# Optimization experiments

Measured on AMD Instinct MI355X. Metric: run time of the kernel, lower is better.

The kernel has to match this reference:

```python
import jax, jax.numpy as jnp
import numpy as np

D = 256
H = 8
DIM = D // H
NL = 8  # number of layers
LAYER_NAMES = ["self", "cross", "self", "cross", "self", "cross", "self", "cross"]
EPS_ATTN = 1e-6
EPS_LN = 1e-5


def setup_inputs() -> dict:
    key = jax.random.key(0)
    ks = jax.random.split(key, 16)
    B, L = 8, 4800
    s = 1.0 / np.sqrt(D)
    inp = {
        "desc0": jax.random.normal(ks[0], (B, L, D), jnp.float32),
        "desc1": jax.random.normal(ks[1], (B, L, D), jnp.float32),
        "mask0": jnp.ones((B, L), jnp.float32),
        "mask1": jnp.ones((B, L), jnp.float32),
        # shared LinearAttention params (one instance reused by all layers)
        "Wq": jax.random.normal(ks[2], (D, D), jnp.float32) * s,
        "bq": jnp.zeros((D,), jnp.float32),
        "Wk": jax.random.normal(ks[3], (D, D), jnp.float32) * s,
        "bk": jnp.zeros((D,), jnp.float32),
        "Wv": jax.random.normal(ks[4], (D, D), jnp.float32) * s,
        "bv": jnp.zeros((D,), jnp.float32),
        "Wm": jax.random.normal(ks[5], (D, D), jnp.float32) * s,
        "bm": jnp.zeros((D,), jnp.float32),
        # per-layer MLP (no bias) and layernorm params, stacked over layers
        "w1": jax.random.normal(ks[6], (NL, D, 2 * D), jnp.float32) * s,
        "w2": jax.random.normal(ks[7], (NL, 2 * D, D), jnp.float32) * (1.0 / np.sqrt(2 * D)),
        "g1": jnp.ones((NL, D), jnp.float32),
        "b1": jnp.zeros((NL, D), jnp.float32),
        "g2": jnp.ones((NL, D), jnp.float32),
        "b2": jnp.zeros((NL, D), jnp.float32),
    }
    return inp


def _layernorm(x, g, b):
    mu = jnp.mean(x, axis=-1, keepdims=True)
    var = jnp.mean(jnp.square(x - mu), axis=-1, keepdims=True)
    return (x - mu) * jax.lax.rsqrt(var + EPS_LN) * g + b


def _linear_attention(q_in, k_in, v_in, qmask, kmask, Wq, bq, Wk, bk, Wv, bv, Wm, bm):
    B, L, _ = q_in.shape
    Q = (q_in @ Wq + bq).reshape(B, -1, H, DIM)
    K = (k_in @ Wk + bk).reshape(B, -1, H, DIM)
    V = (v_in @ Wv + bv).reshape(B, -1, H, DIM)
    Q = jax.nn.elu(Q) + 1.0
    K = jax.nn.elu(K) + 1.0
    Q = Q * qmask[:, :, None, None]
    K = K * kmask[:, :, None, None]
    V = V * kmask[:, :, None, None]
    KV = jnp.einsum("nshd,nshm->nhmd", K, V)          # [B,H,DIM,DIM]
    Z = 1.0 / (jnp.einsum("nlhd,nhd->nlh", Q, K.sum(axis=1)) + EPS_ATTN)
    out = jnp.einsum("nlhd,nhmd,nlh->nlhm", Q, KV, Z)  # [B,L,H,DIM]
    return out.reshape(B, L, D) @ Wm + bm


def _layer(x, source, xmask, smask, Wq, bq, Wk, bk, Wv, bv, Wm, bm, w1, w2, g1, b1, g2, b2):
    msg = _linear_attention(x, source, source, xmask, smask, Wq, bq, Wk, bk, Wv, bv, Wm, bm)
    msg = _layernorm(msg, g1, b1)
    msg = jax.nn.relu(msg @ w1) @ w2
    msg = _layernorm(msg, g2, b2)
    return x + msg


def reference(desc0, desc1, mask0, mask1, Wq, bq, Wk, bk, Wv, bv, Wm, bm, w1, w2, g1, b1, g2, b2):
    attn = (Wq, bq, Wk, bk, Wv, bv, Wm, bm)
    for i, name in enumerate(LAYER_NAMES):
        lp = (w1[i], w2[i], g1[i], b1[i], g2[i], b2[i])
        if name == "self":
            desc0 = _layer(desc0, desc0, mask0, mask0, *attn, *lp)
            desc1 = _layer(desc1, desc1, mask1, mask1, *attn, *lp)
        else:
            desc0 = _layer(desc0, desc1, mask0, mask1, *attn, *lp)
            desc1 = _layer(desc1, desc0, mask1, mask0, *attn, *lp)
    return (desc0, desc1)
```

## Files before the change

kernel.cpp:

```cpp
#include <hip/hip_runtime.h>
#include <hip/hip_bf16.h>

typedef __attribute__((ext_vector_type(8))) short short8;
typedef __attribute__((ext_vector_type(4))) float f32x4;

#define NROWS 38400
#define LSEQ 4800
#define BATCH 8
#define NHEAD 8

__device__ inline float b2f(ushort u) {
  union { ushort s; __hip_bfloat16 h; } c;
  c.s = u;
  return __bfloat162float(c.h);
}
__device__ inline ushort f2b(float f) {
  union { ushort s; __hip_bfloat16 h; } c;
  c.h = __float2bfloat16(f);
  return c.s;
}

__device__ inline void gll16(const void* g, void* l) {
  __builtin_amdgcn_global_load_lds(
      (const __attribute__((address_space(1))) void*)g,
      (__attribute__((address_space(3))) void*)l, 16, 0, 0);
}

__global__ __launch_bounds__(256) void transpose_bf16(
    const float* __restrict__ src, __hip_bfloat16* __restrict__ dst, int R, int C) {
  src += (size_t)blockIdx.z * R * C;
  dst += (size_t)blockIdx.z * R * C;
  __shared__ float tile[32][33];
  int bx = blockIdx.x, by = blockIdx.y;
  int tx = threadIdx.x & 31, ty = threadIdx.x >> 5;
  for (int rr = ty; rr < 32; rr += 8)
    tile[rr][tx] = src[(long)(by * 32 + rr) * C + bx * 32 + tx];
  __syncthreads();
  for (int rr = ty; rr < 32; rr += 8)
    dst[(long)(bx * 32 + rr) * R + by * 32 + tx] = __float2bfloat16(tile[tx][rr]);
}

__global__ __launch_bounds__(256) void init_x(
    const float* __restrict__ d0, const float* __restrict__ d1,
    float* __restrict__ outF, __hip_bfloat16* __restrict__ X0b,
    __hip_bfloat16* __restrict__ X1b, long n) {
  long i = (long)blockIdx.x * 256 + threadIdx.x;
  if (i < n) {
    float a = d0[i], b = d1[i];
    outF[i] = a;
    outF[n + i] = b;
    X0b[i] = __float2bfloat16(a);
    X1b[i] = __float2bfloat16(b);
  }
}

#define BM 128
#define BN 128
#define BKK 64

__global__ __launch_bounds__(256) void gemm_bt(
    const __hip_bfloat16* __restrict__ A, const __hip_bfloat16* __restrict__ Bt,
    const float* __restrict__ bias, const float* __restrict__ rowmask,
    __hip_bfloat16* __restrict__ C, int M, int Nout, int K, int act) {
  __shared__ alignas(16) char smem[128 * 136 * 2];
  __hip_bfloat16 (*As)[64] = (__hip_bfloat16(*)[64])smem;
  __hip_bfloat16 (*Bs)[64] = (__hip_bfloat16(*)[64])(smem + 128 * 64 * 2);
  ushort (*Cs)[136] = (ushort(*)[136])smem;

  int tid = threadIdx.x;
  int wave = tid >> 6, lane = tid & 63;
  int wm = wave & 1, wn = wave >> 1;
  int quad = lane >> 4, l16 = lane & 15;
  long mbase = (long)blockIdx.y * BM;
  long nbase = (long)blockIdx.x * BN;

  int srow = lane >> 3;
  int sck = (lane & 7) ^ srow;
  int cx = l16 & 7;

  f32x4 acc[4][4];
#pragma unroll
  for (int i = 0; i < 4; i++)
#pragma unroll
    for (int j = 0; j < 4; j++) acc[i][j] = (f32x4){0.f, 0.f, 0.f, 0.f};

  for (int kt = 0; kt < K; kt += BKK) {
    __syncthreads();
#pragma unroll
    for (int i = 0; i < 4; i++) {
      int r0 = wave * 32 + i * 8;
      gll16(A + (mbase + r0 + srow) * (long)K + kt + sck * 8, &As[r0][0]);
      gll16(Bt + (nbase + r0 + srow) * (long)K + kt + sck * 8, &Bs[r0][0]);
    }
    __syncthreads();
#pragma unroll
    for (int ks = 0; ks < BKK; ks += 32) {
      short8 af[4], bfr[4];
      int ch = ((ks >> 3) + quad) ^ cx;
#pragma unroll
      for (int mt = 0; mt < 4; mt++)
        af[mt] = *(const short8*)&As[wm * 64 + mt * 16 + l16][ch * 8];
#pragma unroll
      for (int nt = 0; nt < 4; nt++)
        bfr[nt] = *(const short8*)&Bs[wn * 64 + nt * 16 + l16][ch * 8];
#pragma unroll
      for (int mt = 0; mt < 4; mt++)
#pragma unroll
        for (int nt = 0; nt < 4; nt++)
          acc[mt][nt] = __builtin_amdgcn_mfma_f32_16x16x32_bf16(
              af[mt], bfr[nt], acc[mt][nt], 0, 0, 0);
    }
  }

  __syncthreads();
#pragma unroll
  for (int nt = 0; nt < 4; nt++) {
    int colt = wn * 64 + nt * 16 + l16;
    float bv = bias ? bias[nbase + colt] : 0.0f;
#pragma unroll
    for (int mt = 0; mt < 4; mt++) {
      int rowt0 = wm * 64 + mt * 16 + quad * 4;
#pragma unroll
      for (int r = 0; r < 4; r++) {
        int rowt = rowt0 + r;
        float v = acc[mt][nt][r] + bv;
        if (act == 1) v = v > 0.f ? v + 1.f : __expf(v);
        else if (act == 2) v = v > 0.f ? v : 0.f;
        if (rowmask) v *= rowmask[mbase + rowt];
        Cs[rowt][colt] = f2b(v);
      }
    }
  }
  __syncthreads();
#pragma unroll
  for (int it = 0; it < 8; it++) {
    int idx = tid + it * 256;
    int row = idx >> 4, c = idx & 15;
    uint4 v = *(const uint4*)&Cs[row][c * 8];
    *(uint4*)(C + (mbase + row) * (long)Nout + nbase + c * 8) = v;
  }
}

__global__ __launch_bounds__(256) void kv_reduce(
    const __hip_bfloat16* __restrict__ Kp, const __hip_bfloat16* __restrict__ Vp,
    float* __restrict__ KV, float* __restrict__ Ksum) {
  int b = blockIdx.x, h = blockIdx.y, c = blockIdx.z;
  __shared__ float Kl[32][40], Vl[32][40];
  int t = threadIdx.x;
  int lrow = t >> 3, le = (t & 7) * 4;
  int d = t >> 3, mg = t & 7;
  float a0 = 0.f, a1 = 0.f, a2 = 0.f, a3 = 0.f, ks = 0.f;
  int base = c * 480;
  for (int st = 0; st < 15; st++) {
    int s0 = base + st * 32;
    __syncthreads();
    {
      long n = (long)b * LSEQ + s0 + lrow;
      ushort4 ku = *(const ushort4*)(Kp + n * 256 + h * 32 + le);
      ushort4 vu = *(const ushort4*)(Vp + n * 256 + h * 32 + le);
      float4 kf = {b2f(ku.x), b2f(ku.y), b2f(ku.z), b2f(ku.w)};
      float4 vf = {b2f(vu.x), b2f(vu.y), b2f(vu.z), b2f(vu.w)};
      *(float4*)&Kl[lrow][le] = kf;
      *(float4*)&Vl[lrow][le] = vf;
    }
    __syncthreads();
#pragma unroll
    for (int ss = 0; ss < 32; ss++) {
      float kd = Kl[ss][d];
      float4 v4 = *(const float4*)&Vl[ss][mg * 4];
      a0 += kd * v4.x; a1 += kd * v4.y; a2 += kd * v4.z; a3 += kd * v4.w;
      if (mg == 0) ks += kd;
    }
  }
  int bh = b * 8 + h;
  float* p = KV + ((long)bh * 32 + d) * 32 + mg * 4;
  atomicAdd(&p[0], a0); atomicAdd(&p[1], a1);
  atomicAdd(&p[2], a2); atomicAdd(&p[3], a3);
  if (mg == 0) atomicAdd(&Ksum[bh * 32 + d], ks);
}

__global__ __launch_bounds__(256) void attn_out(
    const __hip_bfloat16* __restrict__ Qp, const float* __restrict__ KV,
    const float* __restrict__ Ksum, __hip_bfloat16* __restrict__ O) {
  int b = blockIdx.y, h = blockIdx.z;
  int bh = b * 8 + h;
  __shared__ float KVl[32][36];
  int t = threadIdx.x;
  for (int i = t; i < 1024; i += 256) KVl[i >> 5][i & 31] = KV[((long)bh << 10) + i];
  int lane = t & 63, wave = t >> 6;
  int cg = lane & 7, rs = lane >> 3;
  float4 ksr = *(const float4*)&Ksum[bh * 32 + cg * 4];
  __syncthreads();

  int rowEnd = blockIdx.x * 192 + 192;
  for (int r = blockIdx.x * 192 + wave * 8 + rs; r < rowEnd; r += 32) {
    long n = (long)b * LSEQ + r;
    ushort4 qu = *(const ushort4*)(Qp + n * 256 + h * 32 + cg * 4);
    float q0 = b2f(qu.x), q1 = b2f(qu.y), q2 = b2f(qu.z), q3 = b2f(qu.w);
    float den = q0 * ksr.x + q1 * ksr.y + q2 * ksr.z + q3 * ksr.w;
    den += __shfl_xor(den, 1);
    den += __shfl_xor(den, 2);
    den += __shfl_xor(den, 4);
    float s0 = 0.f, s1 = 0.f, s2 = 0.f, s3 = 0.f;
    int gbase = lane & ~7;
#pragma unroll
    for (int j = 0; j < 8; j++) {
      int src = gbase | j;
      float qa = __shfl(q0, src);
      float qb = __shfl(q1, src);
      float qc = __shfl(q2, src);
      float qd = __shfl(q3, src);
      float4 k0 = *(const float4*)&KVl[j * 4 + 0][cg * 4];
      float4 k1 = *(const float4*)&KVl[j * 4 + 1][cg * 4];
      float4 k2 = *(const float4*)&KVl[j * 4 + 2][cg * 4];
      float4 k3 = *(const float4*)&KVl[j * 4 + 3][cg * 4];
      s0 += qa * k0.x + qb * k1.x + qc * k2.x + qd * k3.x;
      s1 += qa * k0.y + qb * k1.y + qc * k2.y + qd * k3.y;
      s2 += qa * k0.z + qb * k1.z + qc * k2.z + qd * k3.z;
      s3 += qa * k0.w + qb * k1.w + qc * k2.w + qd * k3.w;
    }
    float inv = 1.0f / (den + 1e-6f);
    ushort4 ou = {f2b(s0 * inv), f2b(s1 * inv), f2b(s2 * inv), f2b(s3 * inv)};
    *(ushort4*)(O + n * 256 + h * 32 + cg * 4) = ou;
  }
}

__global__ __launch_bounds__(256) void ln_kernel(
    __hip_bfloat16* __restrict__ X, const float* __restrict__ g,
    const float* __restrict__ bt) {
  int wave = threadIdx.x >> 6, lane = threadIdx.x & 63;
  long row = (long)blockIdx.x * 4 + wave;
  __hip_bfloat16* p = X + row * 256 + lane * 4;
  ushort4 u = *(const ushort4*)p;
  float v[4] = {b2f(u.x), b2f(u.y), b2f(u.z), b2f(u.w)};
  float s = v[0] + v[1] + v[2] + v[3];
  float s2 = v[0] * v[0] + v[1] * v[1] + v[2] * v[2] + v[3] * v[3];
#pragma unroll
  for (int off = 32; off; off >>= 1) {
    s += __shfl_xor(s, off);
    s2 += __shfl_xor(s2, off);
  }
  float mu = s * (1.f / 256.f);
  float var = s2 * (1.f / 256.f) - mu * mu;
  float rs = rsqrtf(var + 1e-5f);
  ushort4 o;
  o.x = f2b((v[0] - mu) * rs * g[lane * 4 + 0] + bt[lane * 4 + 0]);
  o.y = f2b((v[1] - mu) * rs * g[lane * 4 + 1] + bt[lane * 4 + 1]);
  o.z = f2b((v[2] - mu) * rs * g[lane * 4 + 2] + bt[lane * 4 + 2]);
  o.w = f2b((v[3] - mu) * rs * g[lane * 4 + 3] + bt[lane * 4 + 3]);
  *(ushort4*)p = o;
}

__global__ __launch_bounds__(256) void final_kernel(
    const __hip_bfloat16* __restrict__ M2, const float* __restrict__ g,
    const float* __restrict__ bt, float* __restrict__ outF,
    __hip_bfloat16* __restrict__ Xb) {
  int wave = threadIdx.x >> 6, lane = threadIdx.x & 63;
  long row = (long)blockIdx.x * 4 + wave;
  const __hip_bfloat16* p = M2 + row * 256 + lane * 4;
  ushort4 u = *(const ushort4*)p;
  float v[4] = {b2f(u.x), b2f(u.y), b2f(u.z), b2f(u.w)};
  float s = v[0] + v[1] + v[2] + v[3];
  float s2 = v[0] * v[0] + v[1] * v[1] + v[2] * v[2] + v[3] * v[3];
#pragma unroll
  for (int off = 32; off; off >>= 1) {
    s += __shfl_xor(s, off);
    s2 += __shfl_xor(s2, off);
  }
  float mu = s * (1.f / 256.f);
  float var = s2 * (1.f / 256.f) - mu * mu;
  float rs = rsqrtf(var + 1e-5f);
  float* op = outF + row * 256 + lane * 4;
  float4 rv = *(float4*)op;
  float r0 = rv.x + ((v[0] - mu) * rs * g[lane * 4 + 0] + bt[lane * 4 + 0]);
  float r1 = rv.y + ((v[1] - mu) * rs * g[lane * 4 + 1] + bt[lane * 4 + 1]);
  float r2 = rv.z + ((v[2] - mu) * rs * g[lane * 4 + 2] + bt[lane * 4 + 2]);
  float r3 = rv.w + ((v[3] - mu) * rs * g[lane * 4 + 3] + bt[lane * 4 + 3]);
  *(float4*)op = (float4){r0, r1, r2, r3};
  ushort4 xb = {f2b(r0), f2b(r1), f2b(r2), f2b(r3)};
  *(ushort4*)(Xb + row * 256 + lane * 4) = xb;
}

extern "C" void kernel_launch(void* const* d_in, const int* in_sizes, int n_in,
                              void* d_out, int out_size, void* d_ws, size_t ws_size,
                              hipStream_t stream) {
  const float* desc0 = (const float*)d_in[0];
  const float* desc1 = (const float*)d_in[1];
  const float* mask0 = (const float*)d_in[2];
  const float* mask1 = (const float*)d_in[3];
  const float* Wq = (const float*)d_in[4];
  const float* bq = (const float*)d_in[5];
  const float* Wk = (const float*)d_in[6];
  const float* bk = (const float*)d_in[7];
  const float* Wv = (const float*)d_in[8];
  const float* bv = (const float*)d_in[9];
  const float* Wm = (const float*)d_in[10];
  const float* bm = (const float*)d_in[11];
  const float* w1 = (const float*)d_in[12];
  const float* w2 = (const float*)d_in[13];
  const float* g1 = (const float*)d_in[14];
  const float* b1 = (const float*)d_in[15];
  const float* g2 = (const float*)d_in[16];
  const float* b2 = (const float*)d_in[17];

  char* ws = (char*)d_ws;
  auto alloc = [&](size_t bytes) {
    char* p = ws;
    ws += (bytes + 255) & ~(size_t)255;
    return p;
  };
  __hip_bfloat16* WqT = (__hip_bfloat16*)alloc(256 * 256 * 2);
  __hip_bfloat16* WkT = (__hip_bfloat16*)alloc(256 * 256 * 2);
  __hip_bfloat16* WvT = (__hip_bfloat16*)alloc(256 * 256 * 2);
  __hip_bfloat16* WmT = (__hip_bfloat16*)alloc(256 * 256 * 2);
  __hip_bfloat16* w1T = (__hip_bfloat16*)alloc((size_t)8 * 512 * 256 * 2);
  __hip_bfloat16* w2T = (__hip_bfloat16*)alloc((size_t)8 * 256 * 512 * 2);
  __hip_bfloat16* X0b = (__hip_bfloat16*)alloc((size_t)NROWS * 256 * 2);
  __hip_bfloat16* X1b = (__hip_bfloat16*)alloc((size_t)NROWS * 256 * 2);
  __hip_bfloat16* Qb = (__hip_bfloat16*)alloc((size_t)NROWS * 256 * 2);
  __hip_bfloat16* Kb = (__hip_bfloat16*)alloc((size_t)NROWS * 256 * 2);
  __hip_bfloat16* Vb = (__hip_bfloat16*)alloc((size_t)NROWS * 256 * 2);
  __hip_bfloat16* Ab = (__hip_bfloat16*)alloc((size_t)NROWS * 256 * 2);
  __hip_bfloat16* H1b = (__hip_bfloat16*)alloc((size_t)NROWS * 512 * 2);
  float* KVws = (float*)alloc((64 * 1024 + 64 * 32) * 4);
  float* Ksum = KVws + 64 * 1024;

  transpose_bf16<<<dim3(8, 8, 1), 256, 0, stream>>>(Wq, WqT, 256, 256);
  transpose_bf16<<<dim3(8, 8, 1), 256, 0, stream>>>(Wk, WkT, 256, 256);
  transpose_bf16<<<dim3(8, 8, 1), 256, 0, stream>>>(Wv, WvT, 256, 256);
  transpose_bf16<<<dim3(8, 8, 1), 256, 0, stream>>>(Wm, WmT, 256, 256);
  transpose_bf16<<<dim3(16, 8, 8), 256, 0, stream>>>(w1, w1T, 256, 512);
  transpose_bf16<<<dim3(8, 16, 8), 256, 0, stream>>>(w2, w2T, 512, 256);

  long nElem = (long)NROWS * 256;
  init_x<<<(nElem + 255) / 256, 256, 0, stream>>>(desc0, desc1, (float*)d_out,
                                                  X0b, X1b, nElem);

  auto gemm = [&](const __hip_bfloat16* A, const __hip_bfloat16* Bt,
                  const float* bias, const float* rm, __hip_bfloat16* C,
                  int Nout, int K, int act) {
    dim3 grid(Nout / BN, NROWS / BM);
    gemm_bt<<<grid, 256, 0, stream>>>(A, Bt, bias, rm, C, NROWS, Nout, K, act);
  };

  auto layer = [&](int x, int s, int i) {
    __hip_bfloat16* Xx = x ? X1b : X0b;
    __hip_bfloat16* Xs = s ? X1b : X0b;
    const float* mx = x ? mask1 : mask0;
    const float* ms = s ? mask1 : mask0;
    gemm(Xx, WqT, bq, mx, Qb, 256, 256, 1);
    gemm(Xs, WkT, bk, ms, Kb, 256, 256, 1);
    gemm(Xs, WvT, bv, ms, Vb, 256, 256, 0);
    hipMemsetAsync(KVws, 0, (64 * 1024 + 64 * 32) * 4, stream);
    kv_reduce<<<dim3(BATCH, NHEAD, 10), 256, 0, stream>>>(Kb, Vb, KVws, Ksum);
    attn_out<<<dim3(25, BATCH, NHEAD), 256, 0, stream>>>(Qb, KVws, Ksum, Ab);
    gemm(Ab, WmT, bm, nullptr, Kb, 256, 256, 0);
    ln_kernel<<<NROWS / 4, 256, 0, stream>>>(Kb, g1 + i * 256, b1 + i * 256);
    gemm(Kb, w1T + (size_t)i * 512 * 256, nullptr, nullptr, H1b, 512, 256, 2);
    gemm(H1b, w2T + (size_t)i * 256 * 512, nullptr, nullptr, Vb, 256, 512, 0);
    final_kernel<<<NROWS / 4, 256, 0, stream>>>(
        Vb, g2 + i * 256, b2 + i * 256, (float*)d_out + (size_t)x * nElem, Xx);
  };

  for (int i = 0; i < 8; i++) {
    if (i % 2 == 0) {
      layer(0, 0, i);
      layer(1, 1, i);
    } else {
      layer(0, 1, i);
      layer(1, 0, i);
    }
  }
}
```

Measured before the change: 3.549 ms.

## Fuse QKV projections and fold layernorms into GEMM epilogues

Concatenates Wq/Wk/Wv into one transposed weight so Q, K and V are produced by a single GEMM launch for self layers (two launches for cross layers), writing an interleaved 768-wide buffer. The Wm projection and the w2 projection get full-row 64x256 tile GEMMs whose epilogues compute layernorm, and for the final one also the residual add and bf16 copy. This removes the separate ln_kernel and final_kernel passes and their round trips through global memory. It also vectorises init_x. In exchange, the LN GEMMs use a grid of only 600 blocks, and their B tile is reloaded for every 64-row block, which may hurt occupancy and GEMM efficiency.

```diff
diff --git a/kernel.cpp b/kernel.cpp
--- a/kernel.cpp
+++ b/kernel.cpp
@@ -8,6 +8,7 @@
 #define LSEQ 4800
 #define BATCH 8
 #define NHEAD 8
+#define QKV_LD 768
 
 __device__ inline float b2f(ushort u) {
   union { ushort s; __hip_bfloat16 h; } c;
@@ -43,25 +44,26 @@
 __global__ __launch_bounds__(256) void init_x(
     const float* __restrict__ d0, const float* __restrict__ d1,
     float* __restrict__ outF, __hip_bfloat16* __restrict__ X0b,
-    __hip_bfloat16* __restrict__ X1b, long n) {
+    __hip_bfloat16* __restrict__ X1b, long n4) {
   long i = (long)blockIdx.x * 256 + threadIdx.x;
-  if (i < n) {
-    float a = d0[i], b = d1[i];
-    outF[i] = a;
-    outF[n + i] = b;
-    X0b[i] = __float2bfloat16(a);
-    X1b[i] = __float2bfloat16(b);
-  }
-}
-
-#define BM 128
-#define BN 128
-#define BKK 64
-
-__global__ __launch_bounds__(256) void gemm_bt(
+  if (i < n4) {
+    float4 a = ((const float4*)d0)[i];
+    float4 b = ((const float4*)d1)[i];
+    ((float4*)outF)[i] = a;
+    ((float4*)outF)[n4 + i] = b;
+    ushort4 ua = {f2b(a.x), f2b(a.y), f2b(a.z), f2b(a.w)};
+    ushort4 ub = {f2b(b.x), f2b(b.y), f2b(b.z), f2b(b.w)};
+    ((ushort4*)X0b)[i] = ua;
+    ((ushort4*)X1b)[i] = ub;
+  }
+}
+
+__global__ __launch_bounds__(256) void gemm_qkv(
     const __hip_bfloat16* __restrict__ A, const __hip_bfloat16* __restrict__ Bt,
-    const float* __restrict__ bias, const float* __restrict__ rowmask,
-    __hip_bfloat16* __restrict__ C, int M, int Nout, int K, int act) {
+    __hip_bfloat16* __restrict__ C, int col0,
+    const float* __restrict__ bq, const float* __restrict__ bk,
+    const float* __restrict__ bv, const float* __restrict__ mq,
+    const float* __restrict__ mkv) {
   __shared__ alignas(16) char smem[128 * 136 * 2];
   __hip_bfloat16 (*As)[64] = (__hip_bfloat16(*)[64])smem;
   __hip_bfloat16 (*Bs)[64] = (__hip_bfloat16(*)[64])(smem + 128 * 64 * 2);
@@ -71,8 +73,8 @@
   int wave = tid >> 6, lane = tid & 63;
   int wm = wave & 1, wn = wave >> 1;
   int quad = lane >> 4, l16 = lane & 15;
-  long mbase = (long)blockIdx.y * BM;
-  long nbase = (long)blockIdx.x * BN;
+  long mbase = (long)blockIdx.y * 128;
+  int nbase = blockIdx.x * 128;
 
   int srow = lane >> 3;
   int sck = (lane & 7) ^ srow;
@@ -84,17 +86,17 @@
 #pragma unroll
     for (int j = 0; j < 4; j++) acc[i][j] = (f32x4){0.f, 0.f, 0.f, 0.f};
 
-  for (int kt = 0; kt < K; kt += BKK) {
+  for (int kt = 0; kt < 256; kt += 64) {
     __syncthreads();
 #pragma unroll
     for (int i = 0; i < 4; i++) {
       int r0 = wave * 32 + i * 8;
-      gll16(A + (mbase + r0 + srow) * (long)K + kt + sck * 8, &As[r0][0]);
-      gll16(Bt + (nbase + r0 + srow) * (long)K + kt + sck * 8, &Bs[r0][0]);
-    }
-    __syncthreads();
-#pragma unroll
-    for (int ks = 0; ks < BKK; ks += 32) {
+      gll16(A + (mbase + r0 + srow) * 256 + kt + sck * 8, &As[r0][0]);
+      gll16(Bt + (long)(nbase + r0 + srow) * 256 + kt + sck * 8, &Bs[r0][0]);
+    }
+    __syncthreads();
+#pragma unroll
+    for (int ks = 0; ks < 64; ks += 32) {
       short8 af[4], bfr[4];
       int ch = ((ks >> 3) + quad) ^ cx;
 #pragma unroll
@@ -113,20 +115,25 @@
   }
 
   __syncthreads();
+  int gc0 = col0 + nbase;
 #pragma unroll
   for (int nt = 0; nt < 4; nt++) {
     int colt = wn * 64 + nt * 16 + l16;
-    float bv = bias ? bias[nbase + colt] : 0.0f;
+    int gcol = gc0 + colt;
+    int seg = gcol >> 8;
+    int ci = gcol & 255;
+    float bvv = (seg == 0) ? bq[ci] : (seg == 1) ? bk[ci] : bv[ci];
+    const float* mask = (seg == 0) ? mq : mkv;
+    bool doelu = seg < 2;
 #pragma unroll
     for (int mt = 0; mt < 4; mt++) {
       int rowt0 = wm * 64 + mt * 16 + quad * 4;
 #pragma unroll
       for (int r = 0; r < 4; r++) {
         int rowt = rowt0 + r;
-        float v = acc[mt][nt][r] + bv;
-        if (act == 1) v = v > 0.f ? v + 1.f : __expf(v);
-        else if (act == 2) v = v > 0.f ? v : 0.f;
-        if (rowmask) v *= rowmask[mbase + rowt];
+        float v = acc[mt][nt][r] + bvv;
+        if (doelu) v = v > 0.f ? v + 1.f : __expf(v);
+        v *= mask[mbase + rowt];
         Cs[rowt][colt] = f2b(v);
       }
     }
@@ -137,13 +144,331 @@
     int idx = tid + it * 256;
     int row = idx >> 4, c = idx & 15;
     uint4 v = *(const uint4*)&Cs[row][c * 8];
-    *(uint4*)(C + (mbase + row) * (long)Nout + nbase + c * 8) = v;
+    *(uint4*)(C + (mbase + row) * (long)QKV_LD + gc0 + c * 8) = v;
+  }
+}
+
+__global__ __launch_bounds__(256) void gemm_w1(
+    const __hip_bfloat16* __restrict__ A, const __hip_bfloat16* __restrict__ Bt,
+    __hip_bfloat16* __restrict__ C) {
+  __shared__ alignas(16) char smem[128 * 136 * 2];
+  __hip_bfloat16 (*As)[64] = (__hip_bfloat16(*)[64])smem;
+  __hip_bfloat16 (*Bs)[64] = (__hip_bfloat16(*)[64])(smem + 128 * 64 * 2);
+  ushort (*Cs)[136] = (ushort(*)[136])smem;
+
+  int tid = threadIdx.x;
+  int wave = tid >> 6, lane = tid & 63;
+  int wm = wave & 1, wn = wave >> 1;
+  int quad = lane >> 4, l16 = lane & 15;
+  long mbase = (long)blockIdx.y * 128;
+  int nbase = blockIdx.x * 128;
+
+  int srow = lane >> 3;
+  int sck = (lane & 7) ^ srow;
+  int cx = l16 & 7;
+
+  f32x4 acc[4][4];
+#pragma unroll
+  for (int i = 0; i < 4; i++)
+#pragma unroll
+    for (int j = 0; j < 4; j++) acc[i][j] = (f32x4){0.f, 0.f, 0.f, 0.f};
+
+  for (int kt = 0; kt < 256; kt += 64) {
+    __syncthreads();
+#pragma unroll
+    for (int i = 0; i < 4; i++) {
+      int r0 = wave * 32 + i * 8;
+      gll16(A + (mbase + r0 + srow) * 256 + kt + sck * 8, &As[r0][0]);
+      gll16(Bt + (long)(nbase + r0 + srow) * 256 + kt + sck * 8, &Bs[r0][0]);
+    }
+    __syncthreads();
+#pragma unroll
+    for (int ks = 0; ks < 64; ks += 32) {
+      short8 af[4], bfr[4];
+      int ch = ((ks >> 3) + quad) ^ cx;
+#pragma unroll
+      for (int mt = 0; mt < 4; mt++)
+        af[mt] = *(const short8*)&As[wm * 64 + mt * 16 + l16][ch * 8];
+#pragma unroll
+      for (int nt = 0; nt < 4; nt++)
+        bfr[nt] = *(const short8*)&Bs[wn * 64 + nt * 16 + l16][ch * 8];
+#pragma unroll
+      for (int mt = 0; mt < 4; mt++)
+#pragma unroll
+        for (int nt = 0; nt < 4; nt++)
+          acc[mt][nt] = __builtin_amdgcn_mfma_f32_16x16x32_bf16(
+              af[mt], bfr[nt], acc[mt][nt], 0, 0, 0);
+    }
+  }
+
+  __syncthreads();
+#pragma unroll
+  for (int nt = 0; nt < 4; nt++) {
+    int colt = wn * 64 + nt * 16 + l16;
+#pragma unroll
+    for (int mt = 0; mt < 4; mt++) {
+      int rowt0 = wm * 64 + mt * 16 + quad * 4;
+#pragma unroll
+      for (int r = 0; r < 4; r++) {
+        float v = acc[mt][nt][r];
+        Cs[rowt0 + r][colt] = f2b(v > 0.f ? v : 0.f);
+      }
+    }
+  }
+  __syncthreads();
+#pragma unroll
+  for (int it = 0; it < 8; it++) {
+    int idx = tid + it * 256;
+    int row = idx >> 4, c = idx & 15;
+    uint4 v = *(const uint4*)&Cs[row][c * 8];
+    *(uint4*)(C + (mbase + row) * 512L + nbase + c * 8) = v;
+  }
+}
+
+__global__ __launch_bounds__(256) void gemm_ln(
+    const __hip_bfloat16* __restrict__ A, const __hip_bfloat16* __restrict__ Bt,
+    const float* __restrict__ bias, const float* __restrict__ g,
+    const float* __restrict__ bln, __hip_bfloat16* __restrict__ C) {
+  __shared__ alignas(16) char smem[8192 + 32768];
+  __hip_bfloat16 (*As)[64] = (__hip_bfloat16(*)[64])smem;
+  __hip_bfloat16 (*Bs)[64] = (__hip_bfloat16(*)[64])(smem + 8192);
+  ushort (*Cs)[264] = (ushort(*)[264])smem;
+  __shared__ float pS[4][64], pS2[4][64], muA[64], rsA[64];
+
+  int tid = threadIdx.x;
+  int wave = tid >> 6, lane = tid & 63;
+  int wn = wave;
+  int quad = lane >> 4, l16 = lane & 15;
+  long mbase = (long)blockIdx.x * 64;
+
+  int srow = lane >> 3;
+  int sck = (lane & 7) ^ srow;
+  int cx = l16 & 7;
+
+  f32x4 acc[4][4];
+#pragma unroll
+  for (int i = 0; i < 4; i++)
+#pragma unroll
+    for (int j = 0; j < 4; j++) acc[i][j] = (f32x4){0.f, 0.f, 0.f, 0.f};
+
+  for (int kt = 0; kt < 256; kt += 64) {
+    __syncthreads();
+#pragma unroll
+    for (int j = 0; j < 2; j++) {
+      int r0 = wave * 16 + j * 8;
+      gll16(A + (mbase + r0 + srow) * 256 + kt + sck * 8, &As[r0][0]);
+    }
+#pragma unroll
+    for (int j = 0; j < 8; j++) {
+      int r0 = wave * 64 + j * 8;
+      gll16(Bt + (r0 + srow) * 256 + kt + sck * 8, &Bs[r0][0]);
+    }
+    __syncthreads();
+#pragma unroll
+    for (int ks = 0; ks < 64; ks += 32) {
+      short8 af[4], bfr[4];
+      int ch = ((ks >> 3) + quad) ^ cx;
+#pragma unroll
+      for (int mt = 0; mt < 4; mt++)
+        af[mt] = *(const short8*)&As[mt * 16 + l16][ch * 8];
+#pragma unroll
+      for (int nt = 0; nt < 4; nt++)
+        bfr[nt] = *(const short8*)&Bs[wn * 64 + nt * 16 + l16][ch * 8];
+#pragma unroll
+      for (int mt = 0; mt < 4; mt++)
+#pragma unroll
+        for (int nt = 0; nt < 4; nt++)
+          acc[mt][nt] = __builtin_amdgcn_mfma_f32_16x16x32_bf16(
+              af[mt], bfr[nt], acc[mt][nt], 0, 0, 0);
+    }
+  }
+
+  float br[4], gr[4], blr[4];
+#pragma unroll
+  for (int nt = 0; nt < 4; nt++) {
+    int gcol = wn * 64 + nt * 16 + l16;
+    br[nt] = bias[gcol];
+    gr[nt] = g[gcol];
+    blr[nt] = bln[gcol];
+  }
+#pragma unroll
+  for (int mt = 0; mt < 4; mt++)
+#pragma unroll
+    for (int r = 0; r < 4; r++) {
+      float s = 0.f, s2 = 0.f;
+#pragma unroll
+      for (int nt = 0; nt < 4; nt++) {
+        float v = acc[mt][nt][r] + br[nt];
+        s += v;
+        s2 += v * v;
+      }
+      s += __shfl_xor(s, 1);  s2 += __shfl_xor(s2, 1);
+      s += __shfl_xor(s, 2);  s2 += __shfl_xor(s2, 2);
+      s += __shfl_xor(s, 4);  s2 += __shfl_xor(s2, 4);
+      s += __shfl_xor(s, 8);  s2 += __shfl_xor(s2, 8);
+      if (l16 == 0) {
+        int row = mt * 16 + quad * 4 + r;
+        pS[wn][row] = s;
+        pS2[wn][row] = s2;
+      }
+    }
+  __syncthreads();
+  if (tid < 64) {
+    float S = pS[0][tid] + pS[1][tid] + pS[2][tid] + pS[3][tid];
+    float S2 = pS2[0][tid] + pS2[1][tid] + pS2[2][tid] + pS2[3][tid];
+    float mu = S * (1.f / 256.f);
+    float var = S2 * (1.f / 256.f) - mu * mu;
+    muA[tid] = mu;
+    rsA[tid] = rsqrtf(var + 1e-5f);
+  }
+  __syncthreads();
+#pragma unroll
+  for (int mt = 0; mt < 4; mt++)
+#pragma unroll
+    for (int r = 0; r < 4; r++) {
+      int row = mt * 16 + quad * 4 + r;
+      float mu = muA[row], rs = rsA[row];
+#pragma unroll
+      for (int nt = 0; nt < 4; nt++) {
+        float v = acc[mt][nt][r] + br[nt];
+        Cs[row][wn * 64 + nt * 16 + l16] = f2b((v - mu) * rs * gr[nt] + blr[nt]);
+      }
+    }
+  __syncthreads();
+#pragma unroll
+  for (int it = 0; it < 8; it++) {
+    int idx = tid + it * 256;
+    int row = idx >> 5, c = idx & 31;
+    uint4 v = *(const uint4*)&Cs[row][c * 8];
+    *(uint4*)(C + (mbase + row) * 256L + c * 8) = v;
+  }
+}
+
+__global__ __launch_bounds__(256) void gemm_final(
+    const __hip_bfloat16* __restrict__ A, const __hip_bfloat16* __restrict__ Bt,
+    const float* __restrict__ g, const float* __restrict__ bln,
+    float* __restrict__ outF, __hip_bfloat16* __restrict__ Xb) {
+  __shared__ alignas(16) char smem[8192 + 32768];
+  __hip_bfloat16 (*As)[64] = (__hip_bfloat16(*)[64])smem;
+  __hip_bfloat16 (*Bs)[64] = (__hip_bfloat16(*)[64])(smem + 8192);
+  ushort (*Cs)[264] = (ushort(*)[264])smem;
+  __shared__ float pS[4][64], pS2[4][64], muA[64], rsA[64];
+
+  int tid = threadIdx.x;
+  int wave = tid >> 6, lane = tid & 63;
+  int wn = wave;
+  int quad = lane >> 4, l16 = lane & 15;
+  long mbase = (long)blockIdx.x * 64;
+
+  int srow = lane >> 3;
+  int sck = (lane & 7) ^ srow;
+  int cx = l16 & 7;
+
+  f32x4 acc[4][4];
+#pragma unroll
+  for (int i = 0; i < 4; i++)
+#pragma unroll
+    for (int j = 0; j < 4; j++) acc[i][j] = (f32x4){0.f, 0.f, 0.f, 0.f};
+
+  for (int kt = 0; kt < 512; kt += 64) {
+    __syncthreads();
+#pragma unroll
+    for (int j = 0; j < 2; j++) {
+      int r0 = wave * 16 + j * 8;
+      gll16(A + (mbase + r0 + srow) * 512 + kt + sck * 8, &As[r0][0]);
+    }
+#pragma unroll
+    for (int j = 0; j < 8; j++) {
+      int r0 = wave * 64 + j * 8;
+      gll16(Bt + (r0 + srow) * 512L + kt + sck * 8, &Bs[r0][0]);
+    }
+    __syncthreads();
+#pragma unroll
+    for (int ks = 0; ks < 64; ks += 32) {
+      short8 af[4], bfr[4];
+      int ch = ((ks >> 3) + quad) ^ cx;
+#pragma unroll
+      for (int mt = 0; mt < 4; mt++)
+        af[mt] = *(const short8*)&As[mt * 16 + l16][ch * 8];
+#pragma unroll
+      for (int nt = 0; nt < 4; nt++)
+        bfr[nt] = *(const short8*)&Bs[wn * 64 + nt * 16 + l16][ch * 8];
+#pragma unroll
+      for (int mt = 0; mt < 4; mt++)
+#pragma unroll
+        for (int nt = 0; nt < 4; nt++)
+          acc[mt][nt] = __builtin_amdgcn_mfma_f32_16x16x32_bf16(
+              af[mt], bfr[nt], acc[mt][nt], 0, 0, 0);
+    }
+  }
+
+  float gr[4], blr[4];
+#pragma unroll
+  for (int nt = 0; nt < 4; nt++) {
+    int gcol = wn * 64 + nt * 16 + l16;
+    gr[nt] = g[gcol];
+    blr[nt] = bln[gcol];
+  }
+#pragma unroll
+  for (int mt = 0; mt < 4; mt++)
+#pragma unroll
+    for (int r = 0; r < 4; r++) {
+      float s = 0.f, s2 = 0.f;
+#pragma unroll
+      for (int nt = 0; nt < 4; nt++) {
+        float v = acc[mt][nt][r];
+        s += v;
+        s2 += v * v;
+      }
+      s += __shfl_xor(s, 1);  s2 += __shfl_xor(s2, 1);
+      s += __shfl_xor(s, 2);  s2 += __shfl_xor(s2, 2);
+      s += __shfl_xor(s, 4);  s2 += __shfl_xor(s2, 4);
+      s += __shfl_xor(s, 8);  s2 += __shfl_xor(s2, 8);
+      if (l16 == 0) {
+        int row = mt * 16 + quad * 4 + r;
+        pS[wn][row] = s;
+        pS2[wn][row] = s2;
+      }
+    }
+  __syncthreads();
+  if (tid < 64) {
+    float S = pS[0][tid] + pS[1][tid] + pS[2][tid] + pS[3][tid];
+    float S2 = pS2[0][tid] + pS2[1][tid] + pS2[2][tid] + pS2[3][tid];
+    float mu = S * (1.f / 256.f);
+    float var = S2 * (1.f / 256.f) - mu * mu;
+    muA[tid] = mu;
+    rsA[tid] = rsqrtf(var + 1e-5f);
+  }
+  __syncthreads();
+#pragma unroll
+  for (int mt = 0; mt < 4; mt++)
+#pragma unroll
+    for (int r = 0; r < 4; r++) {
+      int row = mt * 16 + quad * 4 + r;
+      float mu = muA[row], rs = rsA[row];
+#pragma unroll
+      for (int nt = 0; nt < 4; nt++) {
+        int gcol = wn * 64 + nt * 16 + l16;
+        float ln = (acc[mt][nt][r] - mu) * rs * gr[nt] + blr[nt];
+        float* op = outF + (mbase + row) * 256 + gcol;
+        float rr = *op + ln;
+        *op = rr;
+        Cs[row][gcol] = f2b(rr);
+      }
+    }
+  __syncthreads();
+#pragma unroll
+  for (int it = 0; it < 8; it++) {
+    int idx = tid + it * 256;
+    int row = idx >> 5, c = idx & 31;
+    uint4 v = *(const uint4*)&Cs[row][c * 8];
+    *(uint4*)(Xb + (mbase + row) * 256L + c * 8) = v;
   }
 }
 
 __global__ __launch_bounds__(256) void kv_reduce(
-    const __hip_bfloat16* __restrict__ Kp, const __hip_bfloat16* __restrict__ Vp,
-    float* __restrict__ KV, float* __restrict__ Ksum) {
+    const __hip_bfloat16* __restrict__ QKV, float* __restrict__ KV,
+    float* __restrict__ Ksum) {
   int b = blockIdx.x, h = blockIdx.y, c = blockIdx.z;
   __shared__ float Kl[32][40], Vl[32][40];
   int t = threadIdx.x;
@@ -156,8 +481,8 @@
     __syncthreads();
     {
       long n = (long)b * LSEQ + s0 + lrow;
-      ushort4 ku = *(const ushort4*)(Kp + n * 256 + h * 32 + le);
-      ushort4 vu = *(const ushort4*)(Vp + n * 256 + h * 32 + le);
+      ushort4 ku = *(const ushort4*)(QKV + n * QKV_LD + 256 + h * 32 + le);
+      ushort4 vu = *(const ushort4*)(QKV + n * QKV_LD + 512 + h * 32 + le);
       float4 kf = {b2f(ku.x), b2f(ku.y), b2f(ku.z), b2f(ku.w)};
       float4 vf = {b2f(vu.x), b2f(vu.y), b2f(vu.z), b2f(vu.w)};
       *(float4*)&Kl[lrow][le] = kf;
@@ -180,7 +505,7 @@
 }
 
 __global__ __launch_bounds__(256) void attn_out(
-    const __hip_bfloat16* __restrict__ Qp, const float* __restrict__ KV,
+    const __hip_bfloat16* __restrict__ QKV, const float* __restrict__ KV,
     const float* __restrict__ Ksum, __hip_bfloat16* __restrict__ O) {
   int b = blockIdx.y, h = blockIdx.z;
   int bh = b * 8 + h;
@@ -195,7 +520,7 @@
   int rowEnd = blockIdx.x * 192 + 192;
   for (int r = blockIdx.x * 192 + wave * 8 + rs; r < rowEnd; r += 32) {
     long n = (long)b * LSEQ + r;
-    ushort4 qu = *(const ushort4*)(Qp + n * 256 + h * 32 + cg * 4);
+    ushort4 qu = *(const ushort4*)(QKV + n * QKV_LD + h * 32 + cg * 4);
     float q0 = b2f(qu.x), q1 = b2f(qu.y), q2 = b2f(qu.z), q3 = b2f(qu.w);
     float den = q0 * ksr.x + q1 * ksr.y + q2 * ksr.z + q3 * ksr.w;
     den += __shfl_xor(den, 1);
@@ -223,62 +548,6 @@
     ushort4 ou = {f2b(s0 * inv), f2b(s1 * inv), f2b(s2 * inv), f2b(s3 * inv)};
     *(ushort4*)(O + n * 256 + h * 32 + cg * 4) = ou;
   }
-}
-
-__global__ __launch_bounds__(256) void ln_kernel(
-    __hip_bfloat16* __restrict__ X, const float* __restrict__ g,
-    const float* __restrict__ bt) {
-  int wave = threadIdx.x >> 6, lane = threadIdx.x & 63;
-  long row = (long)blockIdx.x * 4 + wave;
-  __hip_bfloat16* p = X + row * 256 + lane * 4;
-  ushort4 u = *(const ushort4*)p;
-  float v[4] = {b2f(u.x), b2f(u.y), b2f(u.z), b2f(u.w)};
-  float s = v[0] + v[1] + v[2] + v[3];
-  float s2 = v[0] * v[0] + v[1] * v[1] + v[2] * v[2] + v[3] * v[3];
-#pragma unroll
-  for (int off = 32; off; off >>= 1) {
-    s += __shfl_xor(s, off);
-    s2 += __shfl_xor(s2, off);
-  }
-  float mu = s * (1.f / 256.f);
-  float var = s2 * (1.f / 256.f) - mu * mu;
-  float rs = rsqrtf(var + 1e-5f);
-  ushort4 o;
-  o.x = f2b((v[0] - mu) * rs * g[lane * 4 + 0] + bt[lane * 4 + 0]);
-  o.y = f2b((v[1] - mu) * rs * g[lane * 4 + 1] + bt[lane * 4 + 1]);
-  o.z = f2b((v[2] - mu) * rs * g[lane * 4 + 2] + bt[lane * 4 + 2]);
-  o.w = f2b((v[3] - mu) * rs * g[lane * 4 + 3] + bt[lane * 4 + 3]);
-  *(ushort4*)p = o;
-}
-
-__global__ __launch_bounds__(256) void final_kernel(
-    const __hip_bfloat16* __restrict__ M2, const float* __restrict__ g,
-    const float* __restrict__ bt, float* __restrict__ outF,
-    __hip_bfloat16* __restrict__ Xb) {
-  int wave = threadIdx.x >> 6, lane = threadIdx.x & 63;
-  long row = (long)blockIdx.x * 4 + wave;
-  const __hip_bfloat16* p = M2 + row * 256 + lane * 4;
-  ushort4 u = *(const ushort4*)p;
-  float v[4] = {b2f(u.x), b2f(u.y), b2f(u.z), b2f(u.w)};
-  float s = v[0] + v[1] + v[2] + v[3];
-  float s2 = v[0] * v[0] + v[1] * v[1] + v[2] * v[2] + v[3] * v[3];
-#pragma unroll
-  for (int off = 32; off; off >>= 1) {
-    s += __shfl_xor(s, off);
-    s2 += __shfl_xor(s2, off);
-  }
-  float mu = s * (1.f / 256.f);
-  float var = s2 * (1.f / 256.f) - mu * mu;
-  float rs = rsqrtf(var + 1e-5f);
-  float* op = outF + row * 256 + lane * 4;
-  float4 rv = *(float4*)op;
-  float r0 = rv.x + ((v[0] - mu) * rs * g[lane * 4 + 0] + bt[lane * 4 + 0]);
-  float r1 = rv.y + ((v[1] - mu) * rs * g[lane * 4 + 1] + bt[lane * 4 + 1]);
-  float r2 = rv.z + ((v[2] - mu) * rs * g[lane * 4 + 2] + bt[lane * 4 + 2]);
-  float r3 = rv.w + ((v[3] - mu) * rs * g[lane * 4 + 3] + bt[lane * 4 + 3]);
-  *(float4*)op = (float4){r0, r1, r2, r3};
-  ushort4 xb = {f2b(r0), f2b(r1), f2b(r2), f2b(r3)};
-  *(ushort4*)(Xb + row * 256 + lane * 4) = xb;
 }
 
 extern "C" void kernel_launch(void* const* d_in, const int* in_sizes, int n_in,
@@ -309,57 +578,54 @@
     ws += (bytes + 255) & ~(size_t)255;
     return p;
   };
-  __hip_bfloat16* WqT = (__hip_bfloat16*)alloc(256 * 256 * 2);
-  __hip_bfloat16* WkT = (__hip_bfloat16*)alloc(256 * 256 * 2);
-  __hip_bfloat16* WvT = (__hip_bfloat16*)alloc(256 * 256 * 2);
+  __hip_bfloat16* WqkvT = (__hip_bfloat16*)alloc((size_t)768 * 256 * 2);
   __hip_bfloat16* WmT = (__hip_bfloat16*)alloc(256 * 256 * 2);
   __hip_bfloat16* w1T = (__hip_bfloat16*)alloc((size_t)8 * 512 * 256 * 2);
   __hip_bfloat16* w2T = (__hip_bfloat16*)alloc((size_t)8 * 256 * 512 * 2);
   __hip_bfloat16* X0b = (__hip_bfloat16*)alloc((size_t)NROWS * 256 * 2);
   __hip_bfloat16* X1b = (__hip_bfloat16*)alloc((size_t)NROWS * 256 * 2);
-  __hip_bfloat16* Qb = (__hip_bfloat16*)alloc((size_t)NROWS * 256 * 2);
-  __hip_bfloat16* Kb = (__hip_bfloat16*)alloc((size_t)NROWS * 256 * 2);
-  __hip_bfloat16* Vb = (__hip_bfloat16*)alloc((size_t)NROWS * 256 * 2);
+  __hip_bfloat16* QKV = (__hip_bfloat16*)alloc((size_t)NROWS * QKV_LD * 2);
   __hip_bfloat16* Ab = (__hip_bfloat16*)alloc((size_t)NROWS * 256 * 2);
+  __hip_bfloat16* Mb = (__hip_bfloat16*)alloc((size_t)NROWS * 256 * 2);
   __hip_bfloat16* H1b = (__hip_bfloat16*)alloc((size_t)NROWS * 512 * 2);
   float* KVws = (float*)alloc((64 * 1024 + 64 * 32) * 4);
   float* Ksum = KVws + 64 * 1024;
 
-  transpose_bf16<<<dim3(8, 8, 1), 256, 0, stream>>>(Wq, WqT, 256, 256);
-  transpose_bf16<<<dim3(8, 8, 1), 256, 0, stream>>>(Wk, WkT, 256, 256);
-  transpose_bf16<<<dim3(8, 8, 1), 256, 0, stream>>>(Wv, WvT, 256, 256);
+  transpose_bf16<<<dim3(8, 8, 1), 256, 0, stream>>>(Wq, WqkvT, 256, 256);
+  transpose_bf16<<<dim3(8, 8, 1), 256, 0, stream>>>(Wk, WqkvT + 65536, 256, 256);
+  transpose_bf16<<<dim3(8, 8, 1), 256, 0, stream>>>(Wv, WqkvT + 131072, 256, 256);
   transpose_bf16<<<dim3(8, 8, 1), 256, 0, stream>>>(Wm, WmT, 256, 256);
   transpose_bf16<<<dim3(16, 8, 8), 256, 0, stream>>>(w1, w1T, 256, 512);
   transpose_bf16<<<dim3(8, 16, 8), 256, 0, stream>>>(w2, w2T, 512, 256);
 
   long nElem = (long)NROWS * 256;
-  init_x<<<(nElem + 255) / 256, 256, 0, stream>>>(desc0, desc1, (float*)d_out,
-                                                  X0b, X1b, nElem);
-
-  auto gemm = [&](const __hip_bfloat16* A, const __hip_bfloat16* Bt,
-                  const float* bias, const float* rm, __hip_bfloat16* C,
-                  int Nout, int K, int act) {
-    dim3 grid(Nout / BN, NROWS / BM);
-    gemm_bt<<<grid, 256, 0, stream>>>(A, Bt, bias, rm, C, NROWS, Nout, K, act);
-  };
+  long n4 = nElem / 4;
+  init_x<<<(n4 + 255) / 256, 256, 0, stream>>>(desc0, desc1, (float*)d_out,
+                                               X0b, X1b, n4);
 
   auto layer = [&](int x, int s, int i) {
     __hip_bfloat16* Xx = x ? X1b : X0b;
     __hip_bfloat16* Xs = s ? X1b : X0b;
     const float* mx = x ? mask1 : mask0;
     const float* ms = s ? mask1 : mask0;
-    gemm(Xx, WqT, bq, mx, Qb, 256, 256, 1);
-    gemm(Xs, WkT, bk, ms, Kb, 256, 256, 1);
-    gemm(Xs, WvT, bv, ms, Vb, 256, 256, 0);
+    if (x == s) {
+      gemm_qkv<<<dim3(6, 300), 256, 0, stream>>>(Xx, WqkvT, QKV, 0,
+                                                 bq, bk, bv, mx, ms);
+    } else {
+      gemm_qkv<<<dim3(2, 300), 256, 0, stream>>>(Xx, WqkvT, QKV, 0,
+                                                 bq, bk, bv, mx, ms);
+      gemm_qkv<<<dim3(4, 300), 256, 0, stream>>>(Xs, WqkvT + 65536, QKV, 256,
+                                                 bq, bk, bv, mx, ms);
+    }
     hipMemsetAsync(KVws, 0, (64 * 1024 + 64 * 32) * 4, stream);
-    kv_reduce<<<dim3(BATCH, NHEAD, 10), 256, 0, stream>>>(Kb, Vb, KVws, Ksum);
-    attn_out<<<dim3(25, BATCH, NHEAD), 256, 0, stream>>>(Qb, KVws, Ksum, Ab);
-    gemm(Ab, WmT, bm, nullptr, Kb, 256, 256, 0);
-    ln_kernel<<<NROWS / 4, 256, 0, stream>>>(Kb, g1 + i * 256, b1 + i * 256);
-    gemm(Kb, w1T + (size_t)i * 512 * 256, nullptr, nullptr, H1b, 512, 256, 2);
-    gemm(H1b, w2T + (size_t)i * 256 * 512, nullptr, nullptr, Vb, 256, 512, 0);
-    final_kernel<<<NROWS / 4, 256, 0, stream>>>(
-        Vb, g2 + i * 256, b2 + i * 256, (float*)d_out + (size_t)x * nElem, Xx);
+    kv_reduce<<<dim3(BATCH, NHEAD, 10), 256, 0, stream>>>(QKV, KVws, Ksum);
+    attn_out<<<dim3(25, BATCH, NHEAD), 256, 0, stream>>>(QKV, KVws, Ksum, Ab);
+    gemm_ln<<<NROWS / 64, 256, 0, stream>>>(Ab, WmT, bm, g1 + i * 256,
+                                            b1 + i * 256, Mb);
+    gemm_w1<<<dim3(4, 300), 256, 0, stream>>>(Mb, w1T + (size_t)i * 512 * 256, H1b);
+    gemm_final<<<NROWS / 64, 256, 0, stream>>>(
+        H1b, w2T + (size_t)i * 256 * 512, g2 + i * 256, b2 + i * 256,
+        (float*)d_out + (size_t)x * nElem, Xx);
   };
 
   for (int i = 0; i < 8; i++) {
```

Result: faster. 3.395 ms (-4.4%).
